# Performance work log

Measured on AMD Instinct MI355X. Metric: run time of the kernel, lower is better.

Reference implementation:

```python
import jax, jax.numpy as jnp
import numpy as np

DIM = 3072
NUM_HEADS = 24
HEAD_DIM = DIM // NUM_HEADS  # 128
EPS = 1e-6


def rms_norm(x, scale):
    # x: (..., D); torch F.rms_norm over last dim
    var = jnp.mean(jnp.square(x), axis=-1, keepdims=True)
    return x * jax.lax.rsqrt(var + EPS) * scale


def apply_rope(xq, xk, freqs_cis):
    # xq, xk: (B, H, L, D); freqs_cis: (1, 1, L, D//2, 2, 2)
    B, H, L, D = xq.shape
    xq_ = xq.astype(jnp.float32).reshape(B, H, L, D // 2, 1, 2)
    xk_ = xk.astype(jnp.float32).reshape(B, H, L, D // 2, 1, 2)
    # (1,1,L,D/2,2) * (B,H,L,D/2,1) broadcast -> (B,H,L,D/2,2)
    xq_out = freqs_cis[..., 0] * xq_[..., 0] + freqs_cis[..., 1] * xq_[..., 1]
    xk_out = freqs_cis[..., 0] * xk_[..., 0] + freqs_cis[..., 1] * xk_[..., 1]
    return xq_out.reshape(B, H, L, D).astype(xq.dtype), xk_out.reshape(B, H, L, D).astype(xk.dtype)


def setup_inputs() -> dict:
    key = jax.random.key(0)
    ks = jax.random.split(key, 7)
    B, L = 1, 2048
    x = jax.random.normal(ks[0], (B, L, DIM), dtype=jnp.float32)
    pe = jax.random.normal(ks[1], (1, 1, L, HEAD_DIM // 2, 2, 2), dtype=jnp.float32)
    # parameters (torch nn.Linear layout: weight is (out, in))
    s = 1.0 / np.sqrt(DIM)
    w_qkv = jax.random.uniform(ks[2], (3 * DIM, DIM), minval=-s, maxval=s, dtype=jnp.float32)
    w_proj = jax.random.uniform(ks[3], (DIM, DIM), minval=-s, maxval=s, dtype=jnp.float32)
    b_proj = jax.random.uniform(ks[4], (DIM,), minval=-s, maxval=s, dtype=jnp.float32)
    q_scale = jnp.ones((HEAD_DIM,), dtype=jnp.float32)
    k_scale = jnp.ones((HEAD_DIM,), dtype=jnp.float32)
    return {"x": x, "pe": pe, "w_qkv": w_qkv, "w_proj": w_proj,
            "b_proj": b_proj, "q_scale": q_scale, "k_scale": k_scale}


def reference(x, pe, w_qkv, w_proj, b_proj, q_scale, k_scale):
    B, L, _ = x.shape
    qkv = x @ w_qkv.T  # (B, L, 3*DIM)
    qkv = qkv.reshape(B, L, 3, NUM_HEADS, HEAD_DIM)
    qkv = jnp.transpose(qkv, (2, 0, 3, 1, 4))  # (3, B, H, L, D)
    q, k, v = qkv[0], qkv[1], qkv[2]
    # QKNorm (RMSNorm over head_dim)
    q = rms_norm(q, q_scale)
    k = rms_norm(k, k_scale)
    # RoPE
    q, k = apply_rope(q, k, pe)
    # SDPA: softmax(q k^T / sqrt(D)) v, non-causal
    scores = jnp.einsum("bhqd,bhkd->bhqk", q, k) / np.sqrt(HEAD_DIM).astype(np.float32)
    attn = jax.nn.softmax(scores, axis=-1)
    out = jnp.einsum("bhqk,bhkd->bhqd", attn, v)  # (B, H, L, D)
    out = jnp.transpose(out, (0, 2, 1, 3)).reshape(B, L, DIM)  # B L (H D)
    return out @ w_proj.T + b_proj
```

## Files before the change

### kernel.cpp

```cpp
#include <hip/hip_runtime.h>
#include <hip/hip_bf16.h>

typedef _Float16 f16;
typedef _Float16 f16x2 __attribute__((ext_vector_type(2)));
typedef _Float16 f16x4 __attribute__((ext_vector_type(4)));
typedef _Float16 f16x8 __attribute__((ext_vector_type(8)));
typedef float f32x4 __attribute__((ext_vector_type(4)));

#define L_SEQ 2048
#define DIM 3072
#define NHEAD 24
#define HDIM 128

__device__ __forceinline__ void gll16(const f16* g, f16* l) {
    __builtin_amdgcn_global_load_lds((const __attribute__((address_space(1))) void*)g,
                                     (__attribute__((address_space(3))) void*)l, 16, 0, 0);
}

__global__ __launch_bounds__(256) void cvt3_kernel(const float* __restrict__ s0, f16* __restrict__ d0, int n0,
                                                   const float* __restrict__ s1, f16* __restrict__ d1, int n1,
                                                   const float* __restrict__ s2, f16* __restrict__ d2, int n2) {
    int i = blockIdx.x * blockDim.x + threadIdx.x;
    int stride = gridDim.x * blockDim.x;
    for (int j = i; j < n0; j += stride) {
        float4 v = reinterpret_cast<const float4*>(s0)[j];
        f16x4 o = {(f16)v.x, (f16)v.y, (f16)v.z, (f16)v.w};
        reinterpret_cast<f16x4*>(d0)[j] = o;
    }
    for (int j = i; j < n1; j += stride) {
        float4 v = reinterpret_cast<const float4*>(s1)[j];
        f16x4 o = {(f16)v.x, (f16)v.y, (f16)v.z, (f16)v.w};
        reinterpret_cast<f16x4*>(d1)[j] = o;
    }
    for (int j = i; j < n2; j += stride) {
        float4 v = reinterpret_cast<const float4*>(s2)[j];
        f16x4 o = {(f16)v.x, (f16)v.y, (f16)v.z, (f16)v.w};
        reinterpret_cast<f16x4*>(d2)[j] = o;
    }
}


#define GEMM_BODY_S(T, VM, DO_STAGE)                                                    \
    {                                                                                   \
        asm volatile("s_waitcnt vmcnt(" #VM ")" ::: "memory");                          \
        __builtin_amdgcn_s_barrier();                                                   \
        __builtin_amdgcn_sched_barrier(0);                                              \
        const int slot_ = (T) % 3;                                                      \
        f16x8 af[4], bf[4];                                                             \
        _Pragma("unroll") for (int i = 0; i < 4; i++)                                   \
            af[i] = *reinterpret_cast<const f16x8*>(                                    \
                &As[slot_][(wr + i * 16 + laneM) * 32 + fc16]);                         \
        _Pragma("unroll") for (int j = 0; j < 4; j++)                                   \
            bf[j] = *reinterpret_cast<const f16x8*>(                                    \
                &Bs[slot_][(wc + j * 16 + laneM) * 32 + fc16]);                         \
        if (DO_STAGE) {                                                                 \
            const int t2 = (T) + 2;                                                     \
            const int s2 = t2 % 3;                                                      \
            gll16(Asrc + t2 * 32, &As[s2][dstoff]);                                     \
            gll16(Asrc + (size_t)64 * K + t2 * 32, &As[s2][2048 + dstoff]);             \
            gll16(Bsrc + t2 * 32, &Bs[s2][dstoff]);                                     \
            gll16(Bsrc + (size_t)64 * K + t2 * 32, &Bs[s2][2048 + dstoff]);             \
        }                                                                               \
        __builtin_amdgcn_s_setprio(1);                                                  \
        _Pragma("unroll") for (int i = 0; i < 4; i++)                                   \
            _Pragma("unroll") for (int j = 0; j < 4; j++)                               \
                acc[i][j] =                                                             \
                    __builtin_amdgcn_mfma_f32_16x16x32_f16(af[i], bf[j], acc[i][j],     \
                                                           0, 0, 0);                    \
        __builtin_amdgcn_s_setprio(0);                                                  \
    }

template <int MODE>
__global__ __launch_bounds__(256, 4) void rg128_gemm(const f16* __restrict__ A,
                                                     const f16* __restrict__ B,
                                                     f16* __restrict__ Cf16,
                                                     f16* __restrict__ vT,
                                                     float* __restrict__ Cf32,
                                                     const float* __restrict__ bias,
                                                     int M, int N, int K) {
    __shared__ f16 As[3][128 * 32];
    __shared__ f16 Bs[3][128 * 32];
    const int tid = threadIdx.x;
    const int wid = tid >> 6;
    const int lane = tid & 63;
    const int grp = lane >> 4;
    const int laneM = lane & 15;

    const int nwg = gridDim.x * gridDim.y;
    const int orig = blockIdx.y * gridDim.x + blockIdx.x;
    const int wgid = (orig & 7) * (nwg >> 3) + (orig >> 3);
    const int by = wgid % gridDim.y;
    const int bx = wgid / gridDim.y;
    const int m0 = by * 128;
    const int n0 = bx * 128;

    const int wr = (wid >> 1) * 64;
    const int wc = (wid & 1) * 64;
    const int NT = K >> 5;
    const int fc16 = (grp ^ ((laneM >> 1) & 3)) * 8;

    const int srow = tid >> 2;
    const int scol = (((tid & 3) ^ ((tid >> 3) & 3)) << 3);
    const f16* Asrc = A + (size_t)(m0 + srow) * K + scol;
    const f16* Bsrc = B + (size_t)(n0 + srow) * K + scol;
    const int dstoff = wid * 512;

    const f32x4 vzero = {0.f, 0.f, 0.f, 0.f};
    f32x4 acc[4][4];
#pragma unroll
    for (int i = 0; i < 4; i++)
#pragma unroll
        for (int j = 0; j < 4; j++) acc[i][j] = vzero;

#pragma unroll
    for (int t = 0; t < 2; t++) {
        gll16(Asrc + t * 32, &As[t][dstoff]);
        gll16(Asrc + (size_t)64 * K + t * 32, &As[t][2048 + dstoff]);
        gll16(Bsrc + t * 32, &Bs[t][dstoff]);
        gll16(Bsrc + (size_t)64 * K + t * 32, &Bs[t][2048 + dstoff]);
    }

    int t = 0;
    for (; t < NT - 2; ++t) GEMM_BODY_S(t, 4, true);
    GEMM_BODY_S(t, 4, false); ++t;
    GEMM_BODY_S(t, 0, false);

    if (MODE == 1) {
#pragma unroll
        for (int i = 0; i < 4; i++)
#pragma unroll
            for (int j = 0; j < 4; j++)
#pragma unroll
                for (int r = 0; r < 4; r++) {
                    int row = m0 + wr + i * 16 + grp * 4 + r;
                    int col = n0 + wc + j * 16 + laneM;
                    Cf32[(size_t)row * N + col] = acc[i][j][r] + bias[col];
                }
    } else if (n0 < 2 * DIM) {
#pragma unroll
        for (int i = 0; i < 4; i++)
#pragma unroll
            for (int j = 0; j < 4; j++)
#pragma unroll
                for (int r = 0; r < 4; r++) {
                    int row = m0 + wr + i * 16 + grp * 4 + r;
                    int col = n0 + wc + j * 16 + laneM;
                    Cf16[(size_t)row * N + col] = (f16)acc[i][j][r];
                }
    } else {
#pragma unroll
        for (int i = 0; i < 4; i++)
#pragma unroll
            for (int j = 0; j < 4; j++) {
                int hd = n0 - 2 * DIM + wc + j * 16 + laneM;
                int row0 = m0 + wr + i * 16 + grp * 4;
                f16x4 pk;
#pragma unroll
                for (int r = 0; r < 4; r++) pk[r] = (f16)acc[i][j][r];
                *reinterpret_cast<f16x4*>(&vT[(size_t)hd * L_SEQ + row0]) = pk;
            }
    }
}

__global__ __launch_bounds__(256) void fuse_qk_kernel(const f16* __restrict__ qkv,
                                                      const float* __restrict__ pe,
                                                      const float* __restrict__ qs,
                                                      const float* __restrict__ ks,
                                                      f16* __restrict__ qb,
                                                      f16* __restrict__ kb) {
    const int l = blockIdx.x;
    const int h = blockIdx.y * 4 + (threadIdx.x >> 6);
    const int i = threadIdx.x & 63;
    const f16* row = qkv + (size_t)l * (3 * DIM) + h * HDIM;
    f16x2 qp = *reinterpret_cast<const f16x2*>(row + 2 * i);
    f16x2 kp = *reinterpret_cast<const f16x2*>(row + DIM + 2 * i);
    float q0 = (float)qp[0], q1 = (float)qp[1];
    float k0 = (float)kp[0], k1 = (float)kp[1];
    float sq = q0 * q0 + q1 * q1;
    float sk = k0 * k0 + k1 * k1;
#pragma unroll
    for (int off = 1; off < 64; off <<= 1) {
        sq += __shfl_xor(sq, off);
        sk += __shfl_xor(sk, off);
    }
    const float SCALE = 0.08838834764831845f;
    float rq = rsqrtf(sq * (1.0f / 128.0f) + 1e-6f) * SCALE;
    float rk = rsqrtf(sk * (1.0f / 128.0f) + 1e-6f);
    float4 w = *reinterpret_cast<const float4*>(pe + ((size_t)l * 64 + i) * 4);
    float qa = q0 * rq * qs[2 * i];
    float qbv = q1 * rq * qs[2 * i + 1];
    float ka = k0 * rk * ks[2 * i];
    float kbv = k1 * rk * ks[2 * i + 1];
    f16x2 qo = {(f16)(w.x * qa + w.y * qbv), (f16)(w.z * qa + w.w * qbv)};
    f16x2 ko = {(f16)(w.x * ka + w.y * kbv), (f16)(w.z * ka + w.w * kbv)};
    *reinterpret_cast<f16x2*>(qb + ((size_t)h * L_SEQ + l) * HDIM + 2 * i) = qo;
    *reinterpret_cast<f16x2*>(kb + ((size_t)h * L_SEQ + l) * HDIM + 2 * i) = ko;
}

#define KVBLK 64
#define NSTEP (L_SEQ / KVBLK)

__device__ __forceinline__ void stage_kv(const f16* __restrict__ Kh,
                                         const f16* __restrict__ Vh,
                                         int k0, f16* Kt, f16* Vt, int tid) {
    const int wid = tid >> 6;
    const int krow = tid >> 4;
    const int kcl = (tid & 15) ^ (krow & 7);
    const int vrow = tid >> 3;
    const int vcl = (tid & 7) ^ (vrow & 7);
#pragma unroll
    for (int i = 0; i < 4; i++)
        gll16(Kh + (size_t)(k0 + i * 16 + krow) * HDIM + kcl * 8, Kt + i * 2048 + wid * 512);
#pragma unroll
    for (int i = 0; i < 4; i++)
        gll16(Vh + (size_t)(i * 32 + vrow) * L_SEQ + k0 + vcl * 8, Vt + i * 2048 + wid * 512);
}

__global__ __launch_bounds__(256, 2) void attn_kernel(const f16* __restrict__ qb,
                                                      const f16* __restrict__ kb,
                                                      const f16* __restrict__ vT,
                                                      f16* __restrict__ attnb) {
    __shared__ f16 Kt[2][64 * 128];
    __shared__ f16 Vt[2][128 * 64];
    __shared__ f16 Pl[4][16 * 72];
    const int tid = threadIdx.x;
    const int wid = tid >> 6;
    const int lane = tid & 63;
    const int grp = lane >> 4;
    const int laneM = lane & 15;
    const int h = blockIdx.y;
    const int q0 = blockIdx.x * 64 + wid * 16;
    const f16* Qh = qb + (size_t)h * L_SEQ * HDIM;
    const f16* Kh = kb + (size_t)h * L_SEQ * HDIM;
    const f16* Vh = vT + (size_t)h * HDIM * L_SEQ;

    f16x8 qf[4];
#pragma unroll
    for (int c = 0; c < 4; c++)
        qf[c] = *reinterpret_cast<const f16x8*>(Qh + (size_t)(q0 + laneM) * HDIM + c * 32 + grp * 8);

    const f32x4 vzero = {0.f, 0.f, 0.f, 0.f};
    f32x4 O[8];
#pragma unroll
    for (int f = 0; f < 8; f++) O[f] = vzero;
    float m = -3.0e38f;
    float lsum = 0.f;
    f16* Prow = &Pl[wid][laneM * 72];
    const int swz = laneM & 7;

    stage_kv(Kh, Vh, 0, Kt[0], Vt[0], tid);

    for (int step = 0; step < NSTEP; ++step) {
        const int cur = step & 1;
        __syncthreads();
        if (step + 1 < NSTEP)
            stage_kv(Kh, Vh, (step + 1) * KVBLK, Kt[cur ^ 1], Vt[cur ^ 1], tid);
        const f16* Kc = Kt[cur];
        const f16* Vc = Vt[cur];

        f32x4 s[4];
#pragma unroll
        for (int cc = 0; cc < 4; cc++) s[cc] = vzero;
#pragma unroll
        for (int cc = 0; cc < 4; cc++) {
            f16x8 kf[4];
#pragma unroll
            for (int c = 0; c < 4; c++)
                kf[c] = *reinterpret_cast<const f16x8*>(
                    &Kc[(cc * 16 + laneM) * 128 + (((c * 4 + grp) ^ swz) * 8)]);
#pragma unroll
            for (int c = 0; c < 4; c++)
                s[cc] = __builtin_amdgcn_mfma_f32_16x16x32_f16(kf[c], qf[c], s[cc], 0, 0, 0);
        }

        float pmax = s[0][0];
#pragma unroll
        for (int cc = 0; cc < 4; cc++)
#pragma unroll
            for (int r = 0; r < 4; r++) pmax = fmaxf(pmax, s[cc][r]);
        if (!__all(pmax <= m + 8.0f)) {
            float pm = fmaxf(pmax, __shfl_xor(pmax, 16));
            pm = fmaxf(pm, __shfl_xor(pm, 32));
            float mnew = fmaxf(m, pm);
            float alpha = __expf(m - mnew);
            m = mnew;
            lsum *= alpha;
            float af[4];
#pragma unroll
            for (int r = 0; r < 4; r++) af[r] = __shfl(alpha, grp * 4 + r);
#pragma unroll
            for (int f = 0; f < 8; f++)
#pragma unroll
                for (int r = 0; r < 4; r++) O[f][r] *= af[r];
        }
        float ps = 0.f;
#pragma unroll
        for (int cc = 0; cc < 4; cc++) {
            f16x4 pk;
#pragma unroll
            for (int r = 0; r < 4; r++) {
                float p = __expf(s[cc][r] - m);
                ps += p;
                pk[r] = (f16)p;
            }
            *reinterpret_cast<f16x4*>(Prow + cc * 16 + grp * 4) = pk;
        }
        ps += __shfl_xor(ps, 16);
        ps += __shfl_xor(ps, 32);
        lsum += ps;

#pragma unroll
        for (int z = 0; z < 2; z++) {
            f16x8 pa = *reinterpret_cast<const f16x8*>(Prow + z * 32 + grp * 8);
#pragma unroll
            for (int f = 0; f < 8; f++) {
                f16x8 vf = *reinterpret_cast<const f16x8*>(
                    &Vc[(f * 16 + laneM) * 64 + (((z * 4 + grp) ^ swz) * 8)]);
                O[f] = __builtin_amdgcn_mfma_f32_16x16x32_f16(pa, vf, O[f], 0, 0, 0);
            }
        }
    }

    float li = 1.0f / lsum;
    float lf[4];
#pragma unroll
    for (int r = 0; r < 4; r++) lf[r] = __shfl(li, grp * 4 + r);
#pragma unroll
    for (int f = 0; f < 8; f++)
#pragma unroll
        for (int r = 0; r < 4; r++) {
            int row = q0 + grp * 4 + r;
            attnb[(size_t)row * DIM + h * HDIM + f * 16 + laneM] = (f16)(O[f][r] * lf[r]);
        }
}

extern "C" void kernel_launch(void* const* d_in, const int* in_sizes, int n_in,
                              void* d_out, int out_size, void* d_ws, size_t ws_size,
                              hipStream_t stream) {
    const float* x = (const float*)d_in[0];
    const float* pe = (const float*)d_in[1];
    const float* w_qkv = (const float*)d_in[2];
    const float* w_proj = (const float*)d_in[3];
    const float* b_proj = (const float*)d_in[4];
    const float* q_scale = (const float*)d_in[5];
    const float* k_scale = (const float*)d_in[6];
    float* out = (float*)d_out;

    char* ws = (char*)d_ws;
    f16* xb     = (f16*)(ws + 0);
    f16* wqkvb  = (f16*)(ws + 12582912);
    f16* wprojb = (f16*)(ws + 69206016);
    f16* qkvb   = (f16*)(ws + 88080384);
    f16* qbuf   = (f16*)(ws + 125829120);
    f16* kbuf   = (f16*)(ws + 138412032);
    f16* vT     = (f16*)(ws + 150994944);
    f16* attnb  = (f16*)(ws + 163577856);
    if (ws_size < 176160768) return;

    cvt3_kernel<<<2048, 256, 0, stream>>>(x, xb, (2048 * 3072) / 4,
                                          w_qkv, wqkvb, (9216 * 3072) / 4,
                                          w_proj, wprojb, (3072 * 3072) / 4);

    rg128_gemm<0><<<dim3(72, 16), 256, 0, stream>>>(xb, wqkvb, qkvb, vT, nullptr, nullptr,
                                                    2048, 9216, 3072);
    fuse_qk_kernel<<<dim3(2048, 6), 256, 0, stream>>>(qkvb, pe, q_scale, k_scale, qbuf, kbuf);
    attn_kernel<<<dim3(32, 24), 256, 0, stream>>>(qbuf, kbuf, vT, attnb);
    rg128_gemm<1><<<dim3(24, 16), 256, 0, stream>>>(attnb, wprojb, nullptr, nullptr, out, b_proj,
                                                    2048, 3072, 3072);
}
```

Baseline: 363.1 us.

## Fuse QK RMSNorm and RoPE into QKV GEMM epilogue; deepen proj GEMM pipeline

The separate fuse_qk kernel is removed. Its RMSNorm and RoPE work now runs in the QKV GEMM epilogue: per-row sums of squares are reduced with shuffles and a small shared buffer, and the rotated values are written straight to the per-head Q and K buffers. This drops the intermediate qkv write and read and one kernel launch, at the cost of a barrier and a scattered per-element f16 store pattern in the epilogue. The projection GEMM becomes its own kernel with a 4-stage LDS pipeline (3 tiles in flight) and occupancy hint 2.

```diff
diff --git a/kernel.cpp b/kernel.cpp
--- a/kernel.cpp
+++ b/kernel.cpp
@@ -70,16 +70,18 @@
         __builtin_amdgcn_s_setprio(0);                                                  \
     }
 
-template <int MODE>
-__global__ __launch_bounds__(256, 4) void rg128_gemm(const f16* __restrict__ A,
-                                                     const f16* __restrict__ B,
-                                                     f16* __restrict__ Cf16,
-                                                     f16* __restrict__ vT,
-                                                     float* __restrict__ Cf32,
-                                                     const float* __restrict__ bias,
-                                                     int M, int N, int K) {
+__global__ __launch_bounds__(256, 4) void qkv_gemm(const f16* __restrict__ A,
+                                                   const f16* __restrict__ B,
+                                                   const float* __restrict__ pe,
+                                                   const float* __restrict__ qsc,
+                                                   const float* __restrict__ ksc,
+                                                   f16* __restrict__ qb,
+                                                   f16* __restrict__ kb,
+                                                   f16* __restrict__ vT,
+                                                   int M, int N, int K) {
     __shared__ f16 As[3][128 * 32];
     __shared__ f16 Bs[3][128 * 32];
+    __shared__ float sums[2][128];
     const int tid = threadIdx.x;
     const int wid = tid >> 6;
     const int lane = tid & 63;
@@ -125,29 +127,7 @@
     GEMM_BODY_S(t, 4, false); ++t;
     GEMM_BODY_S(t, 0, false);
 
-    if (MODE == 1) {
-#pragma unroll
-        for (int i = 0; i < 4; i++)
-#pragma unroll
-            for (int j = 0; j < 4; j++)
-#pragma unroll
-                for (int r = 0; r < 4; r++) {
-                    int row = m0 + wr + i * 16 + grp * 4 + r;
-                    int col = n0 + wc + j * 16 + laneM;
-                    Cf32[(size_t)row * N + col] = acc[i][j][r] + bias[col];
-                }
-    } else if (n0 < 2 * DIM) {
-#pragma unroll
-        for (int i = 0; i < 4; i++)
-#pragma unroll
-            for (int j = 0; j < 4; j++)
-#pragma unroll
-                for (int r = 0; r < 4; r++) {
-                    int row = m0 + wr + i * 16 + grp * 4 + r;
-                    int col = n0 + wc + j * 16 + laneM;
-                    Cf16[(size_t)row * N + col] = (f16)acc[i][j][r];
-                }
-    } else {
+    if (n0 >= 2 * DIM) {
 #pragma unroll
         for (int i = 0; i < 4; i++)
 #pragma unroll
@@ -159,42 +139,152 @@
                 for (int r = 0; r < 4; r++) pk[r] = (f16)acc[i][j][r];
                 *reinterpret_cast<f16x4*>(&vT[(size_t)hd * L_SEQ + row0]) = pk;
             }
-    }
-}
-
-__global__ __launch_bounds__(256) void fuse_qk_kernel(const f16* __restrict__ qkv,
-                                                      const float* __restrict__ pe,
-                                                      const float* __restrict__ qs,
-                                                      const float* __restrict__ ks,
-                                                      f16* __restrict__ qb,
-                                                      f16* __restrict__ kb) {
-    const int l = blockIdx.x;
-    const int h = blockIdx.y * 4 + (threadIdx.x >> 6);
-    const int i = threadIdx.x & 63;
-    const f16* row = qkv + (size_t)l * (3 * DIM) + h * HDIM;
-    f16x2 qp = *reinterpret_cast<const f16x2*>(row + 2 * i);
-    f16x2 kp = *reinterpret_cast<const f16x2*>(row + DIM + 2 * i);
-    float q0 = (float)qp[0], q1 = (float)qp[1];
-    float k0 = (float)kp[0], k1 = (float)kp[1];
-    float sq = q0 * q0 + q1 * q1;
-    float sk = k0 * k0 + k1 * k1;
-#pragma unroll
-    for (int off = 1; off < 64; off <<= 1) {
-        sq += __shfl_xor(sq, off);
-        sk += __shfl_xor(sk, off);
-    }
+        return;
+    }
+
+    const bool is_q = (n0 < DIM);
+    const int h = (is_q ? n0 : n0 - DIM) >> 7;
+    const float* sc = is_q ? qsc : ksc;
+    f16* dstb = (is_q ? qb : kb) + (size_t)h * L_SEQ * HDIM;
     const float SCALE = 0.08838834764831845f;
-    float rq = rsqrtf(sq * (1.0f / 128.0f) + 1e-6f) * SCALE;
-    float rk = rsqrtf(sk * (1.0f / 128.0f) + 1e-6f);
-    float4 w = *reinterpret_cast<const float4*>(pe + ((size_t)l * 64 + i) * 4);
-    float qa = q0 * rq * qs[2 * i];
-    float qbv = q1 * rq * qs[2 * i + 1];
-    float ka = k0 * rk * ks[2 * i];
-    float kbv = k1 * rk * ks[2 * i + 1];
-    f16x2 qo = {(f16)(w.x * qa + w.y * qbv), (f16)(w.z * qa + w.w * qbv)};
-    f16x2 ko = {(f16)(w.x * ka + w.y * kbv), (f16)(w.z * ka + w.w * kbv)};
-    *reinterpret_cast<f16x2*>(qb + ((size_t)h * L_SEQ + l) * HDIM + 2 * i) = qo;
-    *reinterpret_cast<f16x2*>(kb + ((size_t)h * L_SEQ + l) * HDIM + 2 * i) = ko;
+
+    float sq[16];
+#pragma unroll
+    for (int i = 0; i < 4; i++)
+#pragma unroll
+        for (int r = 0; r < 4; r++) {
+            float s = 0.f;
+#pragma unroll
+            for (int j = 0; j < 4; j++) s += acc[i][j][r] * acc[i][j][r];
+            sq[i * 4 + r] = s;
+        }
+#pragma unroll
+    for (int off = 1; off < 16; off <<= 1)
+#pragma unroll
+        for (int u = 0; u < 16; u++) sq[u] += __shfl_xor(sq[u], off);
+    if (laneM == 0) {
+#pragma unroll
+        for (int i = 0; i < 4; i++)
+#pragma unroll
+            for (int r = 0; r < 4; r++)
+                sums[wid & 1][wr + i * 16 + grp * 4 + r] = sq[i * 4 + r];
+    }
+    __syncthreads();
+
+#pragma unroll
+    for (int i = 0; i < 4; i++)
+#pragma unroll
+        for (int r = 0; r < 4; r++) {
+            const int rl = wr + i * 16 + grp * 4 + r;
+            const int l = m0 + rl;
+            float tot = sums[0][rl] + sums[1][rl];
+            float rr = rsqrtf(tot * (1.0f / 128.0f) + 1e-6f);
+            if (is_q) rr *= SCALE;
+#pragma unroll
+            for (int j = 0; j < 4; j++) {
+                const int d = wc + j * 16 + laneM;
+                float v = acc[i][j][r] * rr * sc[d];
+                float vp = __shfl_xor(v, 1);
+                float4 w = reinterpret_cast<const float4*>(pe)[(size_t)l * 64 + (d >> 1)];
+                float o = (d & 1) ? (w.z * vp + w.w * v) : (w.x * v + w.y * vp);
+                dstb[(size_t)l * HDIM + d] = (f16)o;
+            }
+        }
+}
+
+#define GEMM_BODY_P(T, VM, DO_STAGE)                                                    \
+    {                                                                                   \
+        asm volatile("s_waitcnt vmcnt(" #VM ")" ::: "memory");                          \
+        __builtin_amdgcn_s_barrier();                                                   \
+        __builtin_amdgcn_sched_barrier(0);                                              \
+        const int slot_ = (T) & 3;                                                      \
+        f16x8 af[4], bf[4];                                                             \
+        _Pragma("unroll") for (int i = 0; i < 4; i++)                                   \
+            af[i] = *reinterpret_cast<const f16x8*>(                                    \
+                &As[slot_][(wr + i * 16 + laneM) * 32 + fc16]);                         \
+        _Pragma("unroll") for (int j = 0; j < 4; j++)                                   \
+            bf[j] = *reinterpret_cast<const f16x8*>(                                    \
+                &Bs[slot_][(wc + j * 16 + laneM) * 32 + fc16]);                         \
+        if (DO_STAGE) {                                                                 \
+            const int t3 = (T) + 3;                                                     \
+            const int s3 = t3 & 3;                                                      \
+            gll16(Asrc + t3 * 32, &As[s3][dstoff]);                                     \
+            gll16(Asrc + (size_t)64 * K + t3 * 32, &As[s3][2048 + dstoff]);             \
+            gll16(Bsrc + t3 * 32, &Bs[s3][dstoff]);                                     \
+            gll16(Bsrc + (size_t)64 * K + t3 * 32, &Bs[s3][2048 + dstoff]);             \
+        }                                                                               \
+        __builtin_amdgcn_s_setprio(1);                                                  \
+        _Pragma("unroll") for (int i = 0; i < 4; i++)                                   \
+            _Pragma("unroll") for (int j = 0; j < 4; j++)                               \
+                acc[i][j] =                                                             \
+                    __builtin_amdgcn_mfma_f32_16x16x32_f16(af[i], bf[j], acc[i][j],     \
+                                                           0, 0, 0);                    \
+        __builtin_amdgcn_s_setprio(0);                                                  \
+    }
+
+__global__ __launch_bounds__(256, 2) void proj_gemm(const f16* __restrict__ A,
+                                                    const f16* __restrict__ B,
+                                                    float* __restrict__ Cf32,
+                                                    const float* __restrict__ bias,
+                                                    int M, int N, int K) {
+    __shared__ f16 As[4][128 * 32];
+    __shared__ f16 Bs[4][128 * 32];
+    const int tid = threadIdx.x;
+    const int wid = tid >> 6;
+    const int lane = tid & 63;
+    const int grp = lane >> 4;
+    const int laneM = lane & 15;
+
+    const int nwg = gridDim.x * gridDim.y;
+    const int orig = blockIdx.y * gridDim.x + blockIdx.x;
+    const int wgid = (orig & 7) * (nwg >> 3) + (orig >> 3);
+    const int by = wgid % gridDim.y;
+    const int bx = wgid / gridDim.y;
+    const int m0 = by * 128;
+    const int n0 = bx * 128;
+
+    const int wr = (wid >> 1) * 64;
+    const int wc = (wid & 1) * 64;
+    const int NT = K >> 5;
+    const int fc16 = (grp ^ ((laneM >> 1) & 3)) * 8;
+
+    const int srow = tid >> 2;
+    const int scol = (((tid & 3) ^ ((tid >> 3) & 3)) << 3);
+    const f16* Asrc = A + (size_t)(m0 + srow) * K + scol;
+    const f16* Bsrc = B + (size_t)(n0 + srow) * K + scol;
+    const int dstoff = wid * 512;
+
+    const f32x4 vzero = {0.f, 0.f, 0.f, 0.f};
+    f32x4 acc[4][4];
+#pragma unroll
+    for (int i = 0; i < 4; i++)
+#pragma unroll
+        for (int j = 0; j < 4; j++) acc[i][j] = vzero;
+
+#pragma unroll
+    for (int t = 0; t < 3; t++) {
+        gll16(Asrc + t * 32, &As[t][dstoff]);
+        gll16(Asrc + (size_t)64 * K + t * 32, &As[t][2048 + dstoff]);
+        gll16(Bsrc + t * 32, &Bs[t][dstoff]);
+        gll16(Bsrc + (size_t)64 * K + t * 32, &Bs[t][2048 + dstoff]);
+    }
+
+    int t = 0;
+    for (; t < NT - 3; ++t) GEMM_BODY_P(t, 8, true);
+    GEMM_BODY_P(t, 8, false); ++t;
+    GEMM_BODY_P(t, 4, false); ++t;
+    GEMM_BODY_P(t, 0, false);
+
+#pragma unroll
+    for (int i = 0; i < 4; i++)
+#pragma unroll
+        for (int j = 0; j < 4; j++)
+#pragma unroll
+            for (int r = 0; r < 4; r++) {
+                int row = m0 + wr + i * 16 + grp * 4 + r;
+                int col = n0 + wc + j * 16 + laneM;
+                Cf32[(size_t)row * N + col] = acc[i][j][r] + bias[col];
+            }
 }
 
 #define KVBLK 64
@@ -350,7 +440,6 @@
     f16* xb     = (f16*)(ws + 0);
     f16* wqkvb  = (f16*)(ws + 12582912);
     f16* wprojb = (f16*)(ws + 69206016);
-    f16* qkvb   = (f16*)(ws + 88080384);
     f16* qbuf   = (f16*)(ws + 125829120);
     f16* kbuf   = (f16*)(ws + 138412032);
     f16* vT     = (f16*)(ws + 150994944);
@@ -361,10 +450,9 @@
                                           w_qkv, wqkvb, (9216 * 3072) / 4,
                                           w_proj, wprojb, (3072 * 3072) / 4);
 
-    rg128_gemm<0><<<dim3(72, 16), 256, 0, stream>>>(xb, wqkvb, qkvb, vT, nullptr, nullptr,
-                                                    2048, 9216, 3072);
-    fuse_qk_kernel<<<dim3(2048, 6), 256, 0, stream>>>(qkvb, pe, q_scale, k_scale, qbuf, kbuf);
+    qkv_gemm<<<dim3(72, 16), 256, 0, stream>>>(xb, wqkvb, pe, q_scale, k_scale,
+                                               qbuf, kbuf, vT, 2048, 9216, 3072);
     attn_kernel<<<dim3(32, 24), 256, 0, stream>>>(qbuf, kbuf, vT, attnb);
-    rg128_gemm<1><<<dim3(24, 16), 256, 0, stream>>>(attnb, wprojb, nullptr, nullptr, out, b_proj,
-                                                    2048, 3072, 3072);
-}
+    proj_gemm<<<dim3(24, 16), 256, 0, stream>>>(attnb, wprojb, out, b_proj,
+                                                2048, 3072, 3072);
+}
```

Result: slower. 454.8 us (+25.3%).
